# Optimization experiments

Measured on AMD Instinct MI355X. Metric: run time of the kernel, lower is better.

The kernel has to match this reference:

```python
import jax, jax.numpy as jnp
import numpy as np

EPS = 0.1
MAX_ITER = 100
THRESH = 0.1


def setup_inputs() -> dict:
    key = jax.random.key(0)
    k1, k2, k3, k4 = jax.random.split(key, 4)
    N, P1, P2, D = 4, 1024, 1024, 16
    x = jax.random.normal(k1, (N, P1, D), dtype=jnp.float32)
    y = jax.random.normal(k2, (N, P2, D), dtype=jnp.float32)
    wx = jax.random.uniform(k3, (N, P1), dtype=jnp.float32)
    wy = jax.random.uniform(k4, (N, P2), dtype=jnp.float32)
    # normalize to probability weights (typical usage for empirical measures)
    wx = wx / jnp.sum(wx, axis=-1, keepdims=True)
    wy = wy / jnp.sum(wy, axis=-1, keepdims=True)
    return {"x": x, "y": y, "wx": wx, "wy": wy}


def _cost_matrix(x, y):
    # |x_i - y_j|^1 summed over feature dim -> [N, P1, P2]
    return jnp.sum(jnp.abs(x[:, :, None, :] - y[:, None, :, :]), axis=-1)


def reference(x, y, wx, wy):
    C = _cost_matrix(x, y)                     # [N, P1, P2]
    mu, nu = wx, wy                            # [N, P1], [N, P2]
    log_mu = jnp.log(mu + 1e-8)
    log_nu = jnp.log(nu + 1e-8)

    def M(u, v):
        # (-C_ij + u_i + v_j) / eps
        return (-C + u[:, :, None] + v[:, None, :]) / EPS

    def step(carry, _):
        u, v, done = carry
        u_new = EPS * (log_mu - jax.nn.logsumexp(M(u, v), axis=-1)) + u
        v_new = EPS * (log_nu - jax.nn.logsumexp(M(u_new, v), axis=-2)) + v
        err = jnp.mean(jnp.sum(jnp.abs(u_new - u), axis=-1))
        # emulate torch's early break: freeze u,v once converged
        u_out = jnp.where(done, u, u_new)
        v_out = jnp.where(done, v, v_new)
        done = done | (err < THRESH)
        return (u_out, v_out, done), None

    u0 = jnp.zeros_like(mu)
    v0 = jnp.zeros_like(nu)
    (u, v, _), _ = jax.lax.scan(step, (u0, v0, jnp.array(False)), None, length=MAX_ITER)

    pi = jnp.exp(M(u, v))                      # transport plan [N, P1, P2]
    cost = jnp.sum(pi * C, axis=(-2, -1))      # [N]  (reduction='none')
    return cost, pi, C
```

## Files before the change

kernel.cpp:

```cpp
#include <hip/hip_runtime.h>

static constexpr int   NB      = 4;
static constexpr int   PP      = 1024;
static constexpr int   DD      = 16;
static constexpr float EPSV    = 0.1f;
static constexpr float KE      = 14.42695041f;
static constexpr float KL      = 0.0693147181f;
static constexpr int   MAXIT   = 100;
static constexpr float THRESHV = 0.1f;

static constexpr int NBLK = 256;
static constexpr int NTHR = 512;
static constexpr unsigned DONEG = 1000000u;

static constexpr int    ERR_F_OFF     = 4352;
static constexpr size_t WS_ZERO_BYTES = 4352 * 4;
static constexpr size_t ERR_BYTES     = 512 * 4;

static constexpr int SNAP_SHIFT = 12;
static constexpr int VSNAP_OFF  = 131072;

__device__ __forceinline__ float fexp2(float v) { return __builtin_amdgcn_exp2f(v); }
__device__ __forceinline__ float flog2(float v) { return __builtin_amdgcn_logf(v); }

__device__ __forceinline__ float aload(const float* p) {
    return __hip_atomic_load(p, __ATOMIC_RELAXED, __HIP_MEMORY_SCOPE_AGENT);
}
__device__ __forceinline__ void astore(float* p, float v) {
    __hip_atomic_store(p, v, __ATOMIC_RELAXED, __HIP_MEMORY_SCOPE_AGENT);
}
__device__ __forceinline__ unsigned aloadu(const unsigned* p) {
    return __hip_atomic_load(p, __ATOMIC_RELAXED, __HIP_MEMORY_SCOPE_AGENT);
}
__device__ __forceinline__ void astoreu(unsigned* p, unsigned v) {
    __hip_atomic_store(p, v, __ATOMIC_RELAXED, __HIP_MEMORY_SCOPE_AGENT);
}
__device__ __forceinline__ float2 aload2(const float* p) {
    unsigned long long v = __hip_atomic_load((const unsigned long long*)p,
                                             __ATOMIC_RELAXED, __HIP_MEMORY_SCOPE_AGENT);
    union { unsigned long long u; float f[2]; } c; c.u = v;
    return make_float2(c.f[0], c.f[1]);
}
__device__ __forceinline__ void astore2(float* p, float a, float b) {
    union { unsigned long long u; float f[2]; } c; c.f[0] = a; c.f[1] = b;
    __hip_atomic_store((unsigned long long*)p, c.u,
                       __ATOMIC_RELAXED, __HIP_MEMORY_SCOPE_AGENT);
}


__device__ __forceinline__ void stage_poll(const unsigned* ws32, int n,
                                           const float* src, unsigned gen,
                                           float* sbuf, int tid) {
    if (tid < 64) {
        const unsigned* sp = ws32 + (n * 64 + tid) * 16;
        const float* cp = src + tid * 16;
        float2 d0, d1, d2, d3, d4, d5, d6, d7;
        bool got = false;
        for (;;) {
            if (!got && aloadu(sp) >= gen) {
                d0 = aload2(cp + 0);  d1 = aload2(cp + 2);
                d2 = aload2(cp + 4);  d3 = aload2(cp + 6);
                d4 = aload2(cp + 8);  d5 = aload2(cp + 10);
                d6 = aload2(cp + 12); d7 = aload2(cp + 14);
                got = true;
            }
            if (__ballot(got) == ~0ull) break;
            __builtin_amdgcn_s_sleep(1);
        }
        const int m = (tid >> 1) & 7;
        *(float4*)&sbuf[4 * ((4 * tid + 0) ^ m)] = make_float4(d0.x, d0.y, d1.x, d1.y);
        *(float4*)&sbuf[4 * ((4 * tid + 1) ^ m)] = make_float4(d2.x, d2.y, d3.x, d3.y);
        *(float4*)&sbuf[4 * ((4 * tid + 2) ^ m)] = make_float4(d4.x, d4.y, d5.x, d5.y);
        *(float4*)&sbuf[4 * ((4 * tid + 3) ^ m)] = make_float4(d6.x, d6.y, d7.x, d7.y);
    }
}

__device__ __forceinline__ void gbar_group(unsigned* ws32, int n, int g, unsigned gen) {
    __syncthreads();
    if (threadIdx.x < 64) {
        if (threadIdx.x == 0) astoreu(ws32 + (n * 64 + g) * 16, gen);
        const unsigned* sp = ws32 + (n * 64 + threadIdx.x) * 16;
        while (__ballot(aloadu(sp) >= gen) != ~0ull)
            __builtin_amdgcn_s_sleep(1);
    }
    __syncthreads();
}

__global__ __launch_bounds__(NTHR, 2)
void sinkhorn_kernel(const float* __restrict__ x, const float* __restrict__ y,
                     const float* __restrict__ wx, const float* __restrict__ wy,
                     float* __restrict__ out, float* __restrict__ ws)
{
    __shared__ float rt[16 * PP];
    __shared__ float sbuf[PP];
    __shared__ float cred[8];
    __shared__ int   Ts;
    __shared__ int   s_ef;
    __shared__ int   s_fired;

    unsigned* ws32  = (unsigned*)ws;
    unsigned* Tslot = ws32 + 4096;
    unsigned* exitf = ws32 + 4104;
    float*    ews   = ws + ERR_F_OFF;

    float* out_cost = out;
    float* out_pi   = out + NB;
    float* out_C    = out + NB + (size_t)NB * PP * PP;

    const int b   = blockIdx.x;
    const int n   = b >> 6;
    const int g   = b & 63;
    const int i0  = g * 16;
    const int w   = threadIdx.x >> 6;
    const int l   = threadIdx.x & 63;
    const int tid = threadIdx.x;

    float* sc = out_C + (size_t)n * PP * PP + SNAP_SHIFT;

    if (tid == 0) { s_ef = 0; s_fired = 0; }

    const int lx = l ^ ((l >> 3) & 7);
    int rv[16];
    #pragma unroll
    for (int k = 0; k < 16; ++k) {
        int s = 16 * k + (l >> 2);
        rv[k] = 4 * (s ^ ((2 * k + (l >> 5)) & 7)) + (l & 3);
    }
    int ea;
    {
        int s = tid >> 1;
        ea = 4 * (s ^ ((tid >> 4) & 7)) + 2 * (tid & 1);
    }

    float4 xr[2][4];
    #pragma unroll
    for (int rr = 0; rr < 2; ++rr) {
        const float4* xp = (const float4*)(x + ((size_t)n * PP + (i0 + 2 * w + rr)) * DD);
        #pragma unroll
        for (int q = 0; q < 4; ++q) xr[rr][q] = xp[q];
    }
    #pragma unroll 4
    for (int k = 0; k < 16; ++k) {
        int j = l + 64 * k;
        const float4* yp = (const float4*)(y + ((size_t)n * PP + j) * DD);
        float4 y0 = yp[0], y1 = yp[1], y2 = yp[2], y3 = yp[3];
        #pragma unroll
        for (int rr = 0; rr < 2; ++rr) {
            float c = fabsf(xr[rr][0].x - y0.x) + fabsf(xr[rr][0].y - y0.y)
                    + fabsf(xr[rr][0].z - y0.z) + fabsf(xr[rr][0].w - y0.w)
                    + fabsf(xr[rr][1].x - y1.x) + fabsf(xr[rr][1].y - y1.y)
                    + fabsf(xr[rr][1].z - y1.z) + fabsf(xr[rr][1].w - y1.w)
                    + fabsf(xr[rr][2].x - y2.x) + fabsf(xr[rr][2].y - y2.y)
                    + fabsf(xr[rr][2].z - y2.z) + fabsf(xr[rr][2].w - y2.w)
                    + fabsf(xr[rr][3].x - y3.x) + fabsf(xr[rr][3].y - y3.y)
                    + fabsf(xr[rr][3].z - y3.z) + fabsf(xr[rr][3].w - y3.w);
            rt[(2 * w + rr) * PP + j] = c;
        }
    }

    float4 yc[2][4];
    #pragma unroll
    for (int c = 0; c < 2; ++c) {
        const float4* yp = (const float4*)(y + ((size_t)n * PP + (i0 + 2 * w + c)) * DD);
        #pragma unroll
        for (int q = 0; q < 4; ++q) yc[c][q] = yp[q];
    }
    float2 c2[16];
    #pragma unroll 4
    for (int k = 0; k < 16; ++k) {
        const float4* xp = (const float4*)(x + ((size_t)n * PP + (l + 64 * k)) * DD);
        float4 x0 = xp[0], x1 = xp[1], x2 = xp[2], x3 = xp[3];
        float cc[2];
        #pragma unroll
        for (int c = 0; c < 2; ++c) {
            cc[c] = fabsf(x0.x - yc[c][0].x) + fabsf(x0.y - yc[c][0].y)
                  + fabsf(x0.z - yc[c][0].z) + fabsf(x0.w - yc[c][0].w)
                  + fabsf(x1.x - yc[c][1].x) + fabsf(x1.y - yc[c][1].y)
                  + fabsf(x1.z - yc[c][1].z) + fabsf(x1.w - yc[c][1].w)
                  + fabsf(x2.x - yc[c][2].x) + fabsf(x2.y - yc[c][2].y)
                  + fabsf(x2.z - yc[c][2].z) + fabsf(x2.w - yc[c][2].w)
                  + fabsf(x3.x - yc[c][3].x) + fabsf(x3.y - yc[c][3].y)
                  + fabsf(x3.z - yc[c][3].z) + fabsf(x3.w - yc[c][3].w);
        }
        c2[k] = make_float2(cc[0], cc[1]);
    }

    float lmu[2], lnu[2];
    #pragma unroll
    for (int rr = 0; rr < 2; ++rr) {
        lmu[rr] = __logf(wx[n * PP + i0 + 2 * w + rr] + 1e-8f);
        lnu[rr] = __logf(wy[n * PP + i0 + 2 * w + rr] + 1e-8f);
    }

    float uprev0 = 0.f, uprev1 = 0.f;

    int last_t = 0;

    #pragma unroll 1
    for (int t = 0; t < MAXIT; ++t) {
        if (t >= 2 && s_ef != 0 && t >= s_ef + 1) break;
        last_t = t;

        if (t == 0) {
            sbuf[ea] = 0.f; sbuf[ea + 1] = 0.f;
        } else {
            stage_poll(ws32, n, sc + VSNAP_OFF + (size_t)(t - 1) * PP,
                       (unsigned)(2 * t), sbuf, tid);
        }
        __syncthreads();

        {
            float4 tt[2][4];
            float m0 = -3.4e38f, m1 = -3.4e38f;
            #pragma unroll
            for (int k = 0; k < 4; ++k) {
                int j = 256 * k + 4 * l;
                float4 v4 = *(const float4*)&sbuf[256 * k + 4 * lx];
                float4 ca = *(const float4*)&rt[(2 * w) * PP + j];
                float4 cb = *(const float4*)&rt[(2 * w + 1) * PP + j];
                tt[0][k] = make_float4(v4.x - ca.x, v4.y - ca.y, v4.z - ca.z, v4.w - ca.w);
                tt[1][k] = make_float4(v4.x - cb.x, v4.y - cb.y, v4.z - cb.z, v4.w - cb.w);
                m0 = fmaxf(m0, fmaxf(fmaxf(tt[0][k].x, tt[0][k].y), fmaxf(tt[0][k].z, tt[0][k].w)));
                m1 = fmaxf(m1, fmaxf(fmaxf(tt[1][k].x, tt[1][k].y), fmaxf(tt[1][k].z, tt[1][k].w)));
            }
            #pragma unroll
            for (int off = 32; off >= 1; off >>= 1) {
                m0 = fmaxf(m0, __shfl_xor(m0, off));
                m1 = fmaxf(m1, __shfl_xor(m1, off));
            }
            float s0 = 0.f, s1 = 0.f;
            #pragma unroll
            for (int k = 0; k < 4; ++k) {
                s0 += fexp2((tt[0][k].x - m0) * KE) + fexp2((tt[0][k].y - m0) * KE)
                    + fexp2((tt[0][k].z - m0) * KE) + fexp2((tt[0][k].w - m0) * KE);
                s1 += fexp2((tt[1][k].x - m1) * KE) + fexp2((tt[1][k].y - m1) * KE)
                    + fexp2((tt[1][k].z - m1) * KE) + fexp2((tt[1][k].w - m1) * KE);
            }
            #pragma unroll
            for (int off = 32; off >= 1; off >>= 1) {
                s0 += __shfl_xor(s0, off);
                s1 += __shfl_xor(s1, off);
            }
            float un0 = EPSV * lmu[0] - (m0 + KL * flog2(s0));
            float un1 = EPSV * lmu[1] - (m1 + KL * flog2(s1));
            if (l == 0) astore2(sc + (size_t)t * PP + i0 + 2 * w, un0, un1);
        }
        __syncthreads();
        if (tid == 0) astoreu(ws32 + (n * 64 + g) * 16, (unsigned)(2 * t + 1));

        stage_poll(ws32, n, sc + (size_t)t * PP, (unsigned)(2 * t + 1), sbuf, tid);
        __syncthreads();

        {
            float up0 = sbuf[ea], up1 = sbuf[ea + 1];
            float we = fabsf(up0 - uprev0) + fabsf(up1 - uprev1);
            uprev0 = up0; uprev1 = up1;
            #pragma unroll
            for (int off = 32; off >= 1; off >>= 1) we += __shfl_xor(we, off);
            if (l == 0) cred[w] = we;
        }

        float dl1[4], dl2[4];
        const bool do_det = (g == 0) && (tid < 64) && (s_fired == 0);
        if (do_det) {
            #pragma unroll
            for (int q = 0; q < NB; ++q) {
                dl1[q] = aload(ews + q * 128 + tid);
                dl2[q] = aload(ews + q * 128 + 64 + tid);
            }
        }

        {
            float tt0[16], tt1[16], m0 = -3.4e38f, m1 = -3.4e38f;
            #pragma unroll
            for (int k = 0; k < 16; ++k) {
                float uu = sbuf[rv[k]];
                tt0[k] = uu - c2[k].x;
                tt1[k] = uu - c2[k].y;
                m0 = fmaxf(m0, tt0[k]);
                m1 = fmaxf(m1, tt1[k]);
            }
            #pragma unroll
            for (int off = 32; off >= 1; off >>= 1) {
                m0 = fmaxf(m0, __shfl_xor(m0, off));
                m1 = fmaxf(m1, __shfl_xor(m1, off));
            }
            float s0 = 0.f, s1 = 0.f;
            #pragma unroll
            for (int k = 0; k < 16; ++k) {
                s0 += fexp2((tt0[k] - m0) * KE);
                s1 += fexp2((tt1[k] - m1) * KE);
            }
            #pragma unroll
            for (int off = 32; off >= 1; off >>= 1) {
                s0 += __shfl_xor(s0, off);
                s1 += __shfl_xor(s1, off);
            }
            float vn0 = EPSV * lnu[0] - (m0 + KL * flog2(s0));
            float vn1 = EPSV * lnu[1] - (m1 + KL * flog2(s1));
            if (l == 0)
                astore2(sc + VSNAP_OFF + (size_t)t * PP + i0 + 2 * w, vn0, vn1);
        }

        __syncthreads();
        if (tid < 64) {
            if (tid == 0) astoreu(ws32 + (n * 64 + g) * 16, (unsigned)(2 * t + 2));
            if (g == 0) {
                float esl = cred[0] + cred[1] + cred[2] + cred[3]
                          + cred[4] + cred[5] + cred[6] + cred[7];
                if (tid == 0) astore(ews + n * 128 + t, esl);
                if (s_fired == 0) {
                    float s1f = 0.f, s2f = 0.f;
                    #pragma unroll
                    for (int q = 0; q < NB; ++q) {
                        float e1 = dl1[q], e2 = dl2[q];
                        if (q == n) {
                            if (tid == t)      e1 = esl;
                            if (64 + tid == t) e2 = esl;
                        }
                        s1f += e1; s2f += e2;
                    }
                    unsigned long long bb = __ballot(s1f < THRESHV * (float)NB)
                                          | __ballot(s2f < THRESHV * (float)NB);
                    if (tid == 0 && bb != 0ull) {
                        astoreu(exitf + n, (unsigned)(t + 1));
                        s_fired = 1;
                    }
                }
            }
        }
        if (tid == 0) s_ef = (int)aloadu(exitf + n);
        __syncthreads();
    }

    {
        const unsigned need = (unsigned)(2 * last_t + 2);
        if (tid < 64) {
            const unsigned* sp = ws32 + (n * 64 + tid) * 16;
            while (__ballot(aloadu(sp) >= need) != ~0ull)
                __builtin_amdgcn_s_sleep(1);
        }
        __syncthreads();
    }

    if (g == 0 && tid == 0) astoreu(ws32 + (n * 64) * 16, DONEG);

    if (b == 0 && tid < 64) {
        for (;;) {
            bool ok = (tid >= 4) || (aloadu(ws32 + tid * 64 * 16) >= DONEG);
            if (__ballot(ok) == ~0ull) break;
            __builtin_amdgcn_s_sleep(2);
        }
        float s1f = aload(ews + 0 * 128 + tid) + aload(ews + 1 * 128 + tid)
                  + aload(ews + 2 * 128 + tid) + aload(ews + 3 * 128 + tid);
        float s2f = aload(ews + 0 * 128 + 64 + tid) + aload(ews + 1 * 128 + 64 + tid)
                  + aload(ews + 2 * 128 + 64 + tid) + aload(ews + 3 * 128 + 64 + tid);
        unsigned long long b1 = __ballot(s1f < THRESHV * (float)NB);
        unsigned long long b2 = __ballot(s2f < THRESHV * (float)NB);
        int T = b1 ? (__ffsll((long long)b1) - 1)
                   : (b2 ? 64 + (__ffsll((long long)b2) - 1) : MAXIT - 1);
        if (tid == 0) astoreu(Tslot, (unsigned)(T + 1));
    }
    if (tid == 0) {
        unsigned tv;
        while ((tv = aloadu(Tslot)) == 0u) __builtin_amdgcn_s_sleep(2);
        Ts = (int)tv - 1;
    }
    __syncthreads();
    const int T = Ts;

    float u_loc[2];
    {
        float2 up = aload2(sc + (size_t)T * PP + i0 + 2 * w);
        u_loc[0] = up.x; u_loc[1] = up.y;
        float2 vp = aload2(sc + VSNAP_OFF + (size_t)T * PP + 2 * tid);
        sbuf[ea] = vp.x; sbuf[ea + 1] = vp.y;
    }
    gbar_group(ws32, n, g, DONEG + 1u);

    float cacc = 0.f;
    #pragma unroll
    for (int rr = 0; rr < 2; ++rr) {
        int r = 2 * w + rr;
        int i = i0 + r;
        float un = u_loc[rr];
        #pragma unroll
        for (int k = 0; k < 4; ++k) {
            int j = 256 * k + 4 * l;
            float4 c4 = *(const float4*)&rt[r * PP + j];
            float4 v4 = *(const float4*)&sbuf[256 * k + 4 * lx];
            float4 p4;
            p4.x = fexp2((un + v4.x - c4.x) * KE);
            p4.y = fexp2((un + v4.y - c4.y) * KE);
            p4.z = fexp2((un + v4.z - c4.z) * KE);
            p4.w = fexp2((un + v4.w - c4.w) * KE);
            *(float4*)&out_pi[((size_t)n * PP + i) * PP + j] = p4;
            *(float4*)&out_C [((size_t)n * PP + i) * PP + j] = c4;
            cacc += p4.x * c4.x + p4.y * c4.y + p4.z * c4.z + p4.w * c4.w;
        }
    }
    #pragma unroll
    for (int off = 32; off >= 1; off >>= 1) cacc += __shfl_xor(cacc, off);
    if (l == 0) cred[w] = cacc;
    __syncthreads();
    if (tid == 0) {
        float s = 0.f;
        #pragma unroll
        for (int q = 0; q < 8; ++q) s += cred[q];
        atomicAdd(&out_cost[n], s);
    }
}

extern "C" void kernel_launch(void* const* d_in, const int* in_sizes, int n_in,
                              void* d_out, int out_size, void* d_ws, size_t ws_size,
                              hipStream_t stream) {
    const float* x  = (const float*)d_in[0];
    const float* y  = (const float*)d_in[1];
    const float* wx = (const float*)d_in[2];
    const float* wy = (const float*)d_in[3];
    float* out = (float*)d_out;
    float* ws  = (float*)d_ws;

    (void)hipMemsetAsync(d_ws, 0, WS_ZERO_BYTES, stream);
    (void)hipMemsetAsync((char*)d_ws + WS_ZERO_BYTES, 0x7f, ERR_BYTES, stream);
    (void)hipMemsetAsync(d_out, 0, NB * sizeof(float), stream);

    hipLaunchKernelGGL(sinkhorn_kernel, dim3(NBLK), dim3(NTHR), 0, stream,
                       x, y, wx, wy, out, ws);
}
```

Baseline: 880.0 us.

## Replace per-phase flag barriers with NaN-sentinel data polling and deferred convergence check

Drops the explicit generation-flag barriers between the u and v half-steps. Blocks now poll the snapshot data directly, which is pre-filled with NaN (0xFF) by a host memset, and proceed as soon as every value is non-NaN. The convergence check moves into the next iteration so it no longer needs its own barrier, and u and v get separate shared buffers. This removes two grid-group synchronisation points per iteration but adds a large memset over the scratch region and relies on fp32 values never being NaN.

```diff
diff --git a/kernel.cpp b/kernel.cpp
--- a/kernel.cpp
+++ b/kernel.cpp
@@ -48,30 +48,36 @@
 }
 
 
-__device__ __forceinline__ void stage_poll(const unsigned* ws32, int n,
-                                           const float* src, unsigned gen,
-                                           float* sbuf, int tid) {
+__device__ __forceinline__ void stage_nan(const float* src, float* dst, int tid) {
     if (tid < 64) {
-        const unsigned* sp = ws32 + (n * 64 + tid) * 16;
         const float* cp = src + tid * 16;
         float2 d0, d1, d2, d3, d4, d5, d6, d7;
         bool got = false;
         for (;;) {
-            if (!got && aloadu(sp) >= gen) {
-                d0 = aload2(cp + 0);  d1 = aload2(cp + 2);
-                d2 = aload2(cp + 4);  d3 = aload2(cp + 6);
-                d4 = aload2(cp + 8);  d5 = aload2(cp + 10);
-                d6 = aload2(cp + 12); d7 = aload2(cp + 14);
-                got = true;
+            if (!got) {
+                float2 s7 = aload2(cp + 14);
+                if ((s7.x == s7.x) & (s7.y == s7.y)) {
+                    d0 = aload2(cp + 0);  d1 = aload2(cp + 2);
+                    d2 = aload2(cp + 4);  d3 = aload2(cp + 6);
+                    d4 = aload2(cp + 8);  d5 = aload2(cp + 10);
+                    d6 = aload2(cp + 12); d7 = s7;
+                    got = (d0.x == d0.x) & (d0.y == d0.y)
+                        & (d1.x == d1.x) & (d1.y == d1.y)
+                        & (d2.x == d2.x) & (d2.y == d2.y)
+                        & (d3.x == d3.x) & (d3.y == d3.y)
+                        & (d4.x == d4.x) & (d4.y == d4.y)
+                        & (d5.x == d5.x) & (d5.y == d5.y)
+                        & (d6.x == d6.x) & (d6.y == d6.y);
+                }
             }
             if (__ballot(got) == ~0ull) break;
             __builtin_amdgcn_s_sleep(1);
         }
         const int m = (tid >> 1) & 7;
-        *(float4*)&sbuf[4 * ((4 * tid + 0) ^ m)] = make_float4(d0.x, d0.y, d1.x, d1.y);
-        *(float4*)&sbuf[4 * ((4 * tid + 1) ^ m)] = make_float4(d2.x, d2.y, d3.x, d3.y);
-        *(float4*)&sbuf[4 * ((4 * tid + 2) ^ m)] = make_float4(d4.x, d4.y, d5.x, d5.y);
-        *(float4*)&sbuf[4 * ((4 * tid + 3) ^ m)] = make_float4(d6.x, d6.y, d7.x, d7.y);
+        *(float4*)&dst[4 * ((4 * tid + 0) ^ m)] = make_float4(d0.x, d0.y, d1.x, d1.y);
+        *(float4*)&dst[4 * ((4 * tid + 1) ^ m)] = make_float4(d2.x, d2.y, d3.x, d3.y);
+        *(float4*)&dst[4 * ((4 * tid + 2) ^ m)] = make_float4(d4.x, d4.y, d5.x, d5.y);
+        *(float4*)&dst[4 * ((4 * tid + 3) ^ m)] = make_float4(d6.x, d6.y, d7.x, d7.y);
     }
 }
 
@@ -92,7 +98,8 @@
                      float* __restrict__ out, float* __restrict__ ws)
 {
     __shared__ float rt[16 * PP];
-    __shared__ float sbuf[PP];
+    __shared__ float ubuf[PP];
+    __shared__ float vbuf[PP];
     __shared__ float cred[8];
     __shared__ int   Ts;
     __shared__ int   s_ef;
@@ -194,20 +201,44 @@
 
     float uprev0 = 0.f, uprev1 = 0.f;
 
-    int last_t = 0;
+    float dl1[NB], dl2[NB];
+    float esl_prev = 3.4e38f;
 
     #pragma unroll 1
     for (int t = 0; t < MAXIT; ++t) {
-        if (t >= 2 && s_ef != 0 && t >= s_ef + 1) break;
-        last_t = t;
+        if (s_ef != 0 && t >= s_ef + 1) break;
 
         if (t == 0) {
-            sbuf[ea] = 0.f; sbuf[ea + 1] = 0.f;
+            ubuf[ea] = 0.f; ubuf[ea + 1] = 0.f;
         } else {
-            stage_poll(ws32, n, sc + VSNAP_OFF + (size_t)(t - 1) * PP,
-                       (unsigned)(2 * t), sbuf, tid);
+            stage_nan(sc + VSNAP_OFF + (size_t)(t - 1) * PP, ubuf, tid);
         }
         __syncthreads();
+
+        if (t >= 1 && g == 0 && tid < 64 && s_fired == 0) {
+            float esl = cred[0] + cred[1] + cred[2] + cred[3]
+                      + cred[4] + cred[5] + cred[6] + cred[7];
+            if (tid == 0) astore(ews + n * 128 + (t - 1), esl);
+            float s1f = 0.f, s2f = 0.f;
+            #pragma unroll
+            for (int q = 0; q < NB; ++q) {
+                float e1 = dl1[q], e2 = dl2[q];
+                if (q == n) {
+                    if (tid == t - 1)           e1 = esl;
+                    else if (tid == t - 2)      e1 = esl_prev;
+                    if (64 + tid == t - 1)      e2 = esl;
+                    else if (64 + tid == t - 2) e2 = esl_prev;
+                }
+                s1f += e1; s2f += e2;
+            }
+            unsigned long long bb = __ballot(s1f < THRESHV * (float)NB)
+                                  | __ballot(s2f < THRESHV * (float)NB);
+            if (bb != 0ull && tid == 0) {
+                astoreu(exitf + n, (unsigned)(t + 1));
+                s_fired = 1;
+            }
+            esl_prev = esl;
+        }
 
         {
             float4 tt[2][4];
@@ -215,7 +246,7 @@
             #pragma unroll
             for (int k = 0; k < 4; ++k) {
                 int j = 256 * k + 4 * l;
-                float4 v4 = *(const float4*)&sbuf[256 * k + 4 * lx];
+                float4 v4 = *(const float4*)&ubuf[256 * k + 4 * lx];
                 float4 ca = *(const float4*)&rt[(2 * w) * PP + j];
                 float4 cb = *(const float4*)&rt[(2 * w + 1) * PP + j];
                 tt[0][k] = make_float4(v4.x - ca.x, v4.y - ca.y, v4.z - ca.z, v4.w - ca.w);
@@ -245,14 +276,14 @@
             float un1 = EPSV * lmu[1] - (m1 + KL * flog2(s1));
             if (l == 0) astore2(sc + (size_t)t * PP + i0 + 2 * w, un0, un1);
         }
+
+        stage_nan(sc + (size_t)t * PP, vbuf, tid);
+        asm volatile("" ::: "memory");
+        if (tid == 0) s_ef = (int)aloadu(exitf + n);
         __syncthreads();
-        if (tid == 0) astoreu(ws32 + (n * 64 + g) * 16, (unsigned)(2 * t + 1));
-
-        stage_poll(ws32, n, sc + (size_t)t * PP, (unsigned)(2 * t + 1), sbuf, tid);
-        __syncthreads();
 
         {
-            float up0 = sbuf[ea], up1 = sbuf[ea + 1];
+            float up0 = vbuf[ea], up1 = vbuf[ea + 1];
             float we = fabsf(up0 - uprev0) + fabsf(up1 - uprev1);
             uprev0 = up0; uprev1 = up1;
             #pragma unroll
@@ -260,21 +291,11 @@
             if (l == 0) cred[w] = we;
         }
 
-        float dl1[4], dl2[4];
-        const bool do_det = (g == 0) && (tid < 64) && (s_fired == 0);
-        if (do_det) {
-            #pragma unroll
-            for (int q = 0; q < NB; ++q) {
-                dl1[q] = aload(ews + q * 128 + tid);
-                dl2[q] = aload(ews + q * 128 + 64 + tid);
-            }
-        }
-
         {
             float tt0[16], tt1[16], m0 = -3.4e38f, m1 = -3.4e38f;
             #pragma unroll
             for (int k = 0; k < 16; ++k) {
-                float uu = sbuf[rv[k]];
+                float uu = vbuf[rv[k]];
                 tt0[k] = uu - c2[k].x;
                 tt1[k] = uu - c2[k].y;
                 m0 = fmaxf(m0, tt0[k]);
@@ -302,45 +323,13 @@
                 astore2(sc + VSNAP_OFF + (size_t)t * PP + i0 + 2 * w, vn0, vn1);
         }
 
-        __syncthreads();
-        if (tid < 64) {
-            if (tid == 0) astoreu(ws32 + (n * 64 + g) * 16, (unsigned)(2 * t + 2));
-            if (g == 0) {
-                float esl = cred[0] + cred[1] + cred[2] + cred[3]
-                          + cred[4] + cred[5] + cred[6] + cred[7];
-                if (tid == 0) astore(ews + n * 128 + t, esl);
-                if (s_fired == 0) {
-                    float s1f = 0.f, s2f = 0.f;
-                    #pragma unroll
-                    for (int q = 0; q < NB; ++q) {
-                        float e1 = dl1[q], e2 = dl2[q];
-                        if (q == n) {
-                            if (tid == t)      e1 = esl;
-                            if (64 + tid == t) e2 = esl;
-                        }
-                        s1f += e1; s2f += e2;
-                    }
-                    unsigned long long bb = __ballot(s1f < THRESHV * (float)NB)
-                                          | __ballot(s2f < THRESHV * (float)NB);
-                    if (tid == 0 && bb != 0ull) {
-                        astoreu(exitf + n, (unsigned)(t + 1));
-                        s_fired = 1;
-                    }
-                }
-            }
-        }
-        if (tid == 0) s_ef = (int)aloadu(exitf + n);
-        __syncthreads();
-    }
-
-    {
-        const unsigned need = (unsigned)(2 * last_t + 2);
-        if (tid < 64) {
-            const unsigned* sp = ws32 + (n * 64 + tid) * 16;
-            while (__ballot(aloadu(sp) >= need) != ~0ull)
-                __builtin_amdgcn_s_sleep(1);
-        }
-        __syncthreads();
+        if (g == 0 && tid < 64 && s_fired == 0) {
+            #pragma unroll
+            for (int q = 0; q < NB; ++q) {
+                dl1[q] = aload(ews + q * 128 + tid);
+                dl2[q] = aload(ews + q * 128 + 64 + tid);
+            }
+        }
     }
 
     if (g == 0 && tid == 0) astoreu(ws32 + (n * 64) * 16, DONEG);
@@ -371,10 +360,14 @@
 
     float u_loc[2];
     {
-        float2 up = aload2(sc + (size_t)T * PP + i0 + 2 * w);
+        const float* upp = sc + (size_t)T * PP + i0 + 2 * w;
+        float2 up;
+        do { up = aload2(upp); } while ((up.x != up.x) | (up.y != up.y));
         u_loc[0] = up.x; u_loc[1] = up.y;
-        float2 vp = aload2(sc + VSNAP_OFF + (size_t)T * PP + 2 * tid);
-        sbuf[ea] = vp.x; sbuf[ea + 1] = vp.y;
+        const float* vpp = sc + VSNAP_OFF + (size_t)T * PP + 2 * tid;
+        float2 vp;
+        do { vp = aload2(vpp); } while ((vp.x != vp.x) | (vp.y != vp.y));
+        vbuf[ea] = vp.x; vbuf[ea + 1] = vp.y;
     }
     gbar_group(ws32, n, g, DONEG + 1u);
 
@@ -388,7 +381,7 @@
         for (int k = 0; k < 4; ++k) {
             int j = 256 * k + 4 * l;
             float4 c4 = *(const float4*)&rt[r * PP + j];
-            float4 v4 = *(const float4*)&sbuf[256 * k + 4 * lx];
+            float4 v4 = *(const float4*)&vbuf[256 * k + 4 * lx];
             float4 p4;
             p4.x = fexp2((un + v4.x - c4.x) * KE);
             p4.y = fexp2((un + v4.y - c4.y) * KE);
@@ -424,6 +417,12 @@
     (void)hipMemsetAsync(d_ws, 0, WS_ZERO_BYTES, stream);
     (void)hipMemsetAsync((char*)d_ws + WS_ZERO_BYTES, 0x7f, ERR_BYTES, stream);
     (void)hipMemsetAsync(d_out, 0, NB * sizeof(float), stream);
+    {
+        size_t out_C_off = ((size_t)NB + (size_t)NB * PP * PP) * sizeof(float);
+        size_t span = (size_t)(NB - 1) * PP * PP * sizeof(float)
+                    + ((size_t)SNAP_SHIFT + VSNAP_OFF + (size_t)MAXIT * PP) * sizeof(float);
+        (void)hipMemsetAsync((char*)d_out + out_C_off, 0xFF, span, stream);
+    }
 
     hipLaunchKernelGGL(sinkhorn_kernel, dim3(NBLK), dim3(NTHR), 0, stream,
                        x, y, wx, wy, out, ws);
```

Result: slower. 1.198 ms (+36.1%).

## Remove end-of-iteration barrier and move convergence detection to a second wavefront

Applied to the files above, without the earlier changes.

Drops the trailing __syncthreads per Sinkhorn iteration. Convergence detection and the error-buffer loads move from wave 0 to wave 1. Wave 1's lane 64 now waits for group 0's half-step flag before reading the exit flag, so all blocks of a batch see the same exit decision without a block-wide barrier. The snapshot area is also no longer offset inside the C output buffer. This cuts one block barrier per iteration in a latency-bound, grid-synchronised loop, but the shared-memory ordering of s_ef, s_fired and cred now relies on the remaining barriers and is more fragile.

```diff
diff --git a/kernel.cpp b/kernel.cpp
--- a/kernel.cpp
+++ b/kernel.cpp
@@ -17,8 +17,7 @@
 static constexpr size_t WS_ZERO_BYTES = 4352 * 4;
 static constexpr size_t ERR_BYTES     = 512 * 4;
 
-static constexpr int SNAP_SHIFT = 12;
-static constexpr int VSNAP_OFF  = 131072;
+static constexpr int VSNAP_OFF = 131072;
 
 __device__ __forceinline__ float fexp2(float v) { return __builtin_amdgcn_exp2f(v); }
 __device__ __forceinline__ float flog2(float v) { return __builtin_amdgcn_logf(v); }
@@ -115,7 +114,7 @@
     const int l   = threadIdx.x & 63;
     const int tid = threadIdx.x;
 
-    float* sc = out_C + (size_t)n * PP * PP + SNAP_SHIFT;
+    float* sc = out_C + (size_t)n * PP * PP;
 
     if (tid == 0) { s_ef = 0; s_fired = 0; }
 
@@ -194,6 +193,8 @@
 
     float uprev0 = 0.f, uprev1 = 0.f;
 
+    float dl1[NB], dl2[NB];
+
     int last_t = 0;
 
     #pragma unroll 1
@@ -248,6 +249,22 @@
         __syncthreads();
         if (tid == 0) astoreu(ws32 + (n * 64 + g) * 16, (unsigned)(2 * t + 1));
 
+        if (tid >= 64 && tid < 128) {
+            if (g == 0 && s_fired == 0) {
+                int dlane = tid - 64;
+                #pragma unroll
+                for (int q = 0; q < NB; ++q) {
+                    dl1[q] = aload(ews + q * 128 + dlane);
+                    dl2[q] = aload(ews + q * 128 + 64 + dlane);
+                }
+            }
+            if (tid == 64) {
+                const unsigned* gsp = ws32 + (n * 64) * 16;
+                while (aloadu(gsp) < (unsigned)(2 * t + 1))
+                    __builtin_amdgcn_s_sleep(1);
+                s_ef = (int)aloadu(exitf + n);
+            }
+        }
         stage_poll(ws32, n, sc + (size_t)t * PP, (unsigned)(2 * t + 1), sbuf, tid);
         __syncthreads();
 
@@ -258,16 +275,6 @@
             #pragma unroll
             for (int off = 32; off >= 1; off >>= 1) we += __shfl_xor(we, off);
             if (l == 0) cred[w] = we;
-        }
-
-        float dl1[4], dl2[4];
-        const bool do_det = (g == 0) && (tid < 64) && (s_fired == 0);
-        if (do_det) {
-            #pragma unroll
-            for (int q = 0; q < NB; ++q) {
-                dl1[q] = aload(ews + q * 128 + tid);
-                dl2[q] = aload(ews + q * 128 + 64 + tid);
-            }
         }
 
         {
@@ -303,34 +310,35 @@
         }
 
         __syncthreads();
-        if (tid < 64) {
-            if (tid == 0) astoreu(ws32 + (n * 64 + g) * 16, (unsigned)(2 * t + 2));
-            if (g == 0) {
+        if (tid == 0) astoreu(ws32 + (n * 64 + g) * 16, (unsigned)(2 * t + 2));
+        if (g == 0) {
+            if (tid == 0) {
+                float es = cred[0] + cred[1] + cred[2] + cred[3]
+                         + cred[4] + cred[5] + cred[6] + cred[7];
+                astore(ews + n * 128 + t, es);
+            }
+            if (tid >= 64 && tid < 128 && s_fired == 0) {
+                int dlane = tid - 64;
                 float esl = cred[0] + cred[1] + cred[2] + cred[3]
                           + cred[4] + cred[5] + cred[6] + cred[7];
-                if (tid == 0) astore(ews + n * 128 + t, esl);
-                if (s_fired == 0) {
-                    float s1f = 0.f, s2f = 0.f;
-                    #pragma unroll
-                    for (int q = 0; q < NB; ++q) {
-                        float e1 = dl1[q], e2 = dl2[q];
-                        if (q == n) {
-                            if (tid == t)      e1 = esl;
-                            if (64 + tid == t) e2 = esl;
-                        }
-                        s1f += e1; s2f += e2;
+                float s1f = 0.f, s2f = 0.f;
+                #pragma unroll
+                for (int q = 0; q < NB; ++q) {
+                    float e1 = dl1[q], e2 = dl2[q];
+                    if (q == n) {
+                        if (dlane == t)      e1 = esl;
+                        if (64 + dlane == t) e2 = esl;
                     }
-                    unsigned long long bb = __ballot(s1f < THRESHV * (float)NB)
-                                          | __ballot(s2f < THRESHV * (float)NB);
-                    if (tid == 0 && bb != 0ull) {
-                        astoreu(exitf + n, (unsigned)(t + 1));
-                        s_fired = 1;
-                    }
+                    s1f += e1; s2f += e2;
                 }
-            }
-        }
-        if (tid == 0) s_ef = (int)aloadu(exitf + n);
-        __syncthreads();
+                unsigned long long bb = __ballot(s1f < THRESHV * (float)NB)
+                                      | __ballot(s2f < THRESHV * (float)NB);
+                if (tid == 64 && bb != 0ull) {
+                    astoreu(exitf + n, (unsigned)(t + 1));
+                    s_fired = 1;
+                }
+            }
+        }
     }
 
     {
```

Result: no change. 884.8 us (+0.5%).
